# Optimization experiments

Measured on AMD Instinct MI355X. Metric: run time of the kernel, lower is better.

Reference implementation:

```python
import jax, jax.numpy as jnp
import numpy as np

DIM_IN = 768
HEADS = 12
DIM_HEAD = 64
SCALE = DIM_HEAD ** (-0.5)


def setup_inputs() -> dict:
    key = jax.random.key(0)
    k_x, k_qkv, k_out = jax.random.split(key, 3)
    B, N = 2, 2048
    x = jax.random.normal(k_x, (B, N, DIM_IN), dtype=jnp.float32)
    # w_qkv: Linear(dim_in, 3*heads*dim_head, bias=False); stored as [in, out] for x @ W
    w_qkv = jax.random.normal(k_qkv, (DIM_IN, HEADS * 3 * DIM_HEAD), dtype=jnp.float32) * (DIM_IN ** -0.5)
    # merge_heads Linear(heads*dim_head, dim_in) with bias
    w_out = jax.random.normal(k_out, (HEADS * DIM_HEAD, DIM_IN), dtype=jnp.float32) * ((HEADS * DIM_HEAD) ** -0.5)
    b_out = jnp.zeros((DIM_IN,), dtype=jnp.float32)
    return {"x": x, "w_qkv": w_qkv, "w_out": w_out, "b_out": b_out}


def reference(x, w_qkv, w_out, b_out):
    B, N, _ = x.shape
    qkv = x @ w_qkv                                   # [B, N, H*3*Dh]
    qkv = qkv.reshape(B, N, HEADS, 3, DIM_HEAD)       # matches torch reshape order
    q = jnp.transpose(qkv[:, :, :, 0, :], (0, 2, 1, 3))  # [B, H, N, Dh]
    k = jnp.transpose(qkv[:, :, :, 1, :], (0, 2, 1, 3))
    v = jnp.transpose(qkv[:, :, :, 2, :], (0, 2, 1, 3))
    scores = jnp.einsum("bhnd,bhmd->bhnm", q, k) * SCALE  # full N x N score matrix
    attn = jax.nn.softmax(scores, axis=-1)
    ctx = jnp.einsum("bhnm,bhmd->bhnd", attn, v)          # [B, H, N, Dh]
    heads = jnp.transpose(ctx, (0, 2, 1, 3)).reshape(B, N, HEADS * DIM_HEAD)
    out = heads @ w_out + b_out                            # dropout is identity at inference
    return out
```

## Files before the change

### kernel.cpp

```cpp
#include <hip/hip_runtime.h>

#define SEQ   2048
#define BATCH 2
#define DIN   768
#define NH    12
#define DH    64
#define QKVN  (NH*3*DH)
#define NBH   (BATCH*NH)
#define QSCALE 0.18033688011112042f

typedef __attribute__((ext_vector_type(8))) short short8;
typedef __attribute__((ext_vector_type(4))) float float4v;

__device__ __forceinline__ ushort f2bf(float f) {
  union { float f; uint u; } v; v.f = f;
  return (ushort)((v.u + 0x7fffu + ((v.u >> 16) & 1u)) >> 16);
}

__device__ __forceinline__ void gld_lds16(const void* g, void* l) {
  __builtin_amdgcn_global_load_lds(
      (__attribute__((address_space(1))) unsigned int*)(g),
      (__attribute__((address_space(3))) unsigned int*)(l), 16, 0, 0);
}

__global__ __launch_bounds__(256) void cvt_all(const float* __restrict__ X,
                                               ushort* __restrict__ Xb,
                                               const float* __restrict__ Wq,
                                               ushort* __restrict__ WqT,
                                               const float* __restrict__ Wo,
                                               ushort* __restrict__ WoT) {
  __shared__ float tile[32][33];
  const int bid = blockIdx.x;
  if (bid < 3072) {
    int i = bid * 256 + threadIdx.x;
    float4 v = ((const float4*)X)[i];
    ushort4 o;
    o.x = f2bf(v.x); o.y = f2bf(v.y); o.z = f2bf(v.z); o.w = f2bf(v.w);
    ((ushort4*)Xb)[i] = o;
    return;
  }
  const float* W; ushort* WT; int Ndim, idx;
  if (bid < 3072 + 1728) { idx = bid - 3072; W = Wq; WT = WqT; Ndim = QKVN; }
  else                   { idx = bid - 4800; W = Wo; WT = WoT; Ndim = DIN;  }
  const int bx = idx % (DIN / 32), by = idx / (DIN / 32);
  const int r0 = bx * 32, c0 = by * 32;
  const int tx = threadIdx.x & 31, tg = threadIdx.x >> 5;
#pragma unroll
  for (int i = 0; i < 4; ++i) {
    int r = tg + i * 8;
    tile[r][tx] = W[(size_t)(r0 + r) * Ndim + c0 + tx];
  }
  __syncthreads();
#pragma unroll
  for (int i = 0; i < 4; ++i) {
    int c = tg + i * 8;
    WT[(size_t)(c0 + c) * DIN + r0 + tx] = f2bf(tile[tx][c]);
  }
}

#define GEMM_CORE(Abf, BT)                                                     \
  __shared__ ushort As[8192];                                                  \
  __shared__ ushort Bs[8192];                                                  \
  const int t = threadIdx.x;                                                   \
  const int lane = t & 63, wid = t >> 6;                                       \
  const int wr = wid >> 1, wc = wid & 1;                                       \
  const int m0 = blockIdx.x * 128, n0 = blockIdx.y * 128;                      \
  float4v acc[4][4] = {};                                                      \
  for (int k0 = 0; k0 < DIN; k0 += 64) {                                       \
    __syncthreads();                                                           \
    _Pragma("unroll")                                                          \
    for (int i = 0; i < 4; ++i) {                                              \
      int s   = t + i * 256;                                                   \
      int sub = s >> 7, kss = (s >> 6) & 1, l = s & 63;                        \
      int row = sub * 16 + (l & 15);                                           \
      int kc  = kss * 32 + (l >> 4) * 8;                                       \
      int lb  = (i * 256 + wid * 64) * 8;           \
      gld_lds16(&Abf[(size_t)(m0 + row) * DIN + k0 + kc], &As[lb]);            \
      gld_lds16(&BT[(size_t)(n0 + row) * DIN + k0 + kc], &Bs[lb]);             \
    }                                                                          \
    __syncthreads();                                                           \
    _Pragma("unroll")                                                          \
    for (int ks = 0; ks < 2; ++ks) {                                           \
      short8 a[4], b[4];                                                       \
      _Pragma("unroll")                                                        \
      for (int mi = 0; mi < 4; ++mi)                                           \
        a[mi] = *(const short8*)&As[(((wr * 4 + mi) * 2 + ks) * 64 + lane) * 8];\
      _Pragma("unroll")                                                        \
      for (int ni = 0; ni < 4; ++ni)                                           \
        b[ni] = *(const short8*)&Bs[(((wc * 4 + ni) * 2 + ks) * 64 + lane) * 8];\
      _Pragma("unroll")                                                        \
      for (int mi = 0; mi < 4; ++mi)                                           \
        _Pragma("unroll")                                                      \
        for (int ni = 0; ni < 4; ++ni)                                         \
          acc[mi][ni] = __builtin_amdgcn_mfma_f32_16x16x32_bf16(               \
              a[mi], b[ni], acc[mi][ni], 0, 0, 0);                             \
    }                                                                          \
  }

__global__ __launch_bounds__(256) void gemm_qkv(const ushort* __restrict__ Abf,
                                                const ushort* __restrict__ BT,
                                                ushort* __restrict__ Q,
                                                ushort* __restrict__ K,
                                                ushort* __restrict__ Vt) {
  GEMM_CORE(Abf, BT)
  __syncthreads();
  ushort* scr = &As[wid * 1024];
  const int eL = lane & 15, eH = lane >> 4;
  const int cb64  = n0 + wc * 64;
  const int h     = cb64 / 192;
  const int which = (cb64 % 192) / 64;
  const int mbase = m0 + wr * 64;
  if (which == 2) {
#pragma unroll
    for (int ni = 0; ni < 4; ++ni) {
      const int d0 = ni * 16 + eL;
#pragma unroll
      for (int mi = 0; mi < 4; ++mi) {
        const int mrow = mbase + mi * 16 + eH * 4;
        const int bb = mrow >> 11, n = mrow & (SEQ - 1);
        const int bhv = bb * NH + h;
        ushort4 pk;
        pk.x = f2bf(acc[mi][ni][0]); pk.y = f2bf(acc[mi][ni][1]);
        pk.z = f2bf(acc[mi][ni][2]); pk.w = f2bf(acc[mi][ni][3]);
        *(ushort4*)&Vt[((size_t)bhv * DH + d0) * SEQ + n] = pk;
      }
    }
  } else {
    ushort* dst = (which == 0) ? Q : K;
    const float sc = (which == 0) ? QSCALE : 1.0f;
    const int rr = lane >> 2;
    const int rb = (lane & 3) ^ (rr >> 2);
    const int roff = rr * 64 + rb * 16;
#pragma unroll
    for (int mi = 0; mi < 4; ++mi) {
      const int mrow = mbase + mi * 16;
      const int bb = mrow >> 11, nb = mrow & (SEQ - 1);
#pragma unroll
      for (int ni = 0; ni < 4; ++ni) {
        const int sb = ((ni ^ eH) & 3) * 16;
#pragma unroll
        for (int r = 0; r < 4; ++r)
          scr[(eH * 4 + r) * 64 + sb + eL] = f2bf(acc[mi][ni][r] * sc);
      }
      asm volatile("s_waitcnt lgkmcnt(0)" ::: "memory");
      short8 v0 = *(const short8*)&scr[roff];
      short8 v1 = *(const short8*)&scr[roff + 8];
      ushort* gp = dst + ((size_t)(bb * NH + h) * SEQ + nb) * DH + lane * 16;
      *(short8*)&gp[0] = v0;
      *(short8*)&gp[8] = v1;
      asm volatile("s_waitcnt lgkmcnt(0)" ::: "memory");
    }
  }
}

__global__ __launch_bounds__(256) void gemm_out(const ushort* __restrict__ Abf,
                                                const ushort* __restrict__ BT,
                                                const float* __restrict__ bias,
                                                float* __restrict__ Out) {
  GEMM_CORE(Abf, BT)
#pragma unroll
  for (int ni = 0; ni < 4; ++ni) {
    const int c = n0 + wc * 64 + ni * 16 + (lane & 15);
    const float bv = bias[c];
#pragma unroll
    for (int mi = 0; mi < 4; ++mi) {
      const int mrow = m0 + wr * 64 + mi * 16 + (lane >> 4) * 4;
#pragma unroll
      for (int r = 0; r < 4; ++r)
        Out[(size_t)(mrow + r) * DIN + c] = acc[mi][ni][r] + bv;
    }
  }
}

__global__ __launch_bounds__(256) void attn(const ushort* __restrict__ Q,
                                            const ushort* __restrict__ K,
                                            const ushort* __restrict__ Vt,
                                            ushort* __restrict__ CTX) {
  __shared__ ushort Ks[2][4096];
  __shared__ ushort Vs[2][4096];
  __shared__ ushort ps[4][1024];
  const int t = threadIdx.x, lane = t & 63, wid = t >> 6;
  const int lo = lane & 15, hi = lane >> 4;
  const int bid = blockIdx.x;
  const int bh = bid % NBH;
  const int q0 = (bid / NBH) * 64 + wid * 16;
  const size_t base = (size_t)bh * SEQ * DH;
  ushort* myps = ps[wid];

  int kvoff[4][2];
#pragma unroll
  for (int ns = 0; ns < 4; ++ns)
#pragma unroll
    for (int ks = 0; ks < 2; ++ks) {
      int row = ns * 16 + lo;
      kvoff[ns][ks] = (row * 128 + ks * 64 + hi * 16) ^ ((row & 7) << 4);
    }
  int pwoff[4], proff[2];
#pragma unroll
  for (int ns = 0; ns < 4; ++ns)
    pwoff[ns] = (lo * 128 + ns * 32 + hi * 8) ^ ((lo & 7) << 4);
#pragma unroll
  for (int ks = 0; ks < 2; ++ks)
    proff[ks] = (lo * 128 + ks * 64 + hi * 16) ^ ((lo & 7) << 4);

  const int c0i = t, c1i = t + 256;
  const int g0 = c0i ^ ((c0i >> 3) & 7), g1 = c1i ^ ((c1i >> 3) & 7);
  const int lb0 = (wid * 64) * 8, lb1 = (256 + wid * 64) * 8;
  const ushort* kp0 = K + base + g0 * 8;
  const ushort* kp1 = K + base + g1 * 8;
  const ushort* vp0 = Vt + (size_t)bh * DH * SEQ + (size_t)(g0 >> 3) * SEQ + (g0 & 7) * 8;
  const ushort* vp1 = Vt + (size_t)bh * DH * SEQ + (size_t)(g1 >> 3) * SEQ + (g1 & 7) * 8;

  short8 qf[2];
#pragma unroll
  for (int ks = 0; ks < 2; ++ks)
    qf[ks] = *(const short8*)&Q[base + (size_t)(q0 + lo) * DH + ks * 32 + hi * 8];

  float4v Ot[4] = {};
  float mrun = -1e30f, lrun = 0.f;

  gld_lds16(kp0, &Ks[0][lb0]);
  gld_lds16(kp1, &Ks[0][lb1]);
  gld_lds16(vp0, &Vs[0][lb0]);
  gld_lds16(vp1, &Vs[0][lb1]);
  kp0 += 64 * DH; kp1 += 64 * DH; vp0 += 64; vp1 += 64;
  __syncthreads();

  const int NT = SEQ / 64;
  for (int kt = 0; kt < NT; ++kt) {
    const int cur = kt & 1, nb = cur ^ 1;
    const char* Kl = (const char*)&Ks[cur][0];
    const char* Vl = (const char*)&Vs[cur][0];
    if (kt + 1 < NT) {
      gld_lds16(kp0, &Ks[nb][lb0]);
      gld_lds16(kp1, &Ks[nb][lb1]);
      gld_lds16(vp0, &Vs[nb][lb0]);
      gld_lds16(vp1, &Vs[nb][lb1]);
      kp0 += 64 * DH; kp1 += 64 * DH; vp0 += 64; vp1 += 64;
    }
    float4v st[4];
#pragma unroll
    for (int ns = 0; ns < 4; ++ns) {
      st[ns] = (float4v){0.f, 0.f, 0.f, 0.f};
#pragma unroll
      for (int ks = 0; ks < 2; ++ks) {
        short8 kf = *(const short8*)(Kl + kvoff[ns][ks]);
        st[ns] = __builtin_amdgcn_mfma_f32_16x16x32_bf16(kf, qf[ks], st[ns], 0, 0, 0);
      }
    }
    float mx = fmaxf(fmaxf(fmaxf(st[0][0], st[0][1]), fmaxf(st[0][2], st[0][3])),
                     fmaxf(fmaxf(st[1][0], st[1][1]), fmaxf(st[1][2], st[1][3])));
    mx = fmaxf(mx, fmaxf(fmaxf(fmaxf(st[2][0], st[2][1]), fmaxf(st[2][2], st[2][3])),
                         fmaxf(fmaxf(st[3][0], st[3][1]), fmaxf(st[3][2], st[3][3]))));
    mx = fmaxf(mx, __shfl_xor(mx, 16));
    mx = fmaxf(mx, __shfl_xor(mx, 32));
    if (!__all(mx <= mrun + 8.0f)) {
      float mnew  = fmaxf(mrun, mx);
      float alpha = exp2f(mrun - mnew);
      lrun *= alpha;
#pragma unroll
      for (int ns = 0; ns < 4; ++ns)
#pragma unroll
        for (int r = 0; r < 4; ++r) Ot[ns][r] *= alpha;
      mrun = mnew;
    }
    float p[4][4];
    float rs = 0.f;
#pragma unroll
    for (int ns = 0; ns < 4; ++ns)
#pragma unroll
      for (int r = 0; r < 4; ++r) {
        p[ns][r] = exp2f(st[ns][r] - mrun);
        rs += p[ns][r];
      }
    rs += __shfl_xor(rs, 16);
    rs += __shfl_xor(rs, 32);
    lrun += rs;
#pragma unroll
    for (int ns = 0; ns < 4; ++ns) {
      uint2 d2;
      d2.x = __builtin_amdgcn_perm(__float_as_uint(p[ns][1]),
                                   __float_as_uint(p[ns][0]), 0x07060302u);
      d2.y = __builtin_amdgcn_perm(__float_as_uint(p[ns][3]),
                                   __float_as_uint(p[ns][2]), 0x07060302u);
      *(uint2*)((char*)myps + pwoff[ns]) = d2;
    }
    asm volatile("s_waitcnt lgkmcnt(0)" ::: "memory");
    short8 pf[2];
#pragma unroll
    for (int ks = 0; ks < 2; ++ks)
      pf[ks] = *(const short8*)((char*)myps + proff[ks]);
    __builtin_amdgcn_s_setprio(1);
#pragma unroll
    for (int ns = 0; ns < 4; ++ns)
#pragma unroll
      for (int ks = 0; ks < 2; ++ks) {
        short8 vf = *(const short8*)(Vl + kvoff[ns][ks]);
        Ot[ns] = __builtin_amdgcn_mfma_f32_16x16x32_bf16(vf, pf[ks], Ot[ns], 0, 0, 0);
      }
    __builtin_amdgcn_s_setprio(0);
    __syncthreads();
  }
  const int bb = bh / NH, h = bh % NH;
  const float inv = 1.0f / lrun;
  const int n = q0 + lo;
#pragma unroll
  for (int ns = 0; ns < 4; ++ns) {
    ushort4 o;
    o.x = f2bf(Ot[ns][0] * inv); o.y = f2bf(Ot[ns][1] * inv);
    o.z = f2bf(Ot[ns][2] * inv); o.w = f2bf(Ot[ns][3] * inv);
    *(ushort4*)&CTX[(size_t)(bb * SEQ + n) * DIN + h * DH + ns * 16 + hi * 4] = o;
  }
}

extern "C" void kernel_launch(void* const* d_in, const int* in_sizes, int n_in,
                              void* d_out, int out_size, void* d_ws, size_t ws_size,
                              hipStream_t stream) {
  const float* x     = (const float*)d_in[0];
  const float* w_qkv = (const float*)d_in[1];
  const float* w_out = (const float*)d_in[2];
  const float* b_out = (const float*)d_in[3];
  float* out = (float*)d_out;

  ushort* ws = (ushort*)d_ws;
  const size_t nX   = (size_t)BATCH * SEQ * DIN;
  const size_t nWq  = (size_t)DIN * QKVN;
  const size_t nWo  = (size_t)DIN * DIN;
  const size_t nQKV = (size_t)BATCH * NH * SEQ * DH;

  ushort* xb   = ws;
  ushort* wqT  = xb + nX;
  ushort* woT  = wqT + nWq;
  ushort* Qb   = woT + nWo;
  ushort* Kb   = Qb + nQKV;
  ushort* Vt   = Kb + nQKV;
  ushort* CTX  = Vt + nQKV;

  cvt_all<<<dim3(5376), 256, 0, stream>>>(x, xb, w_qkv, wqT, w_out, woT);
  gemm_qkv<<<dim3(BATCH * SEQ / 128, QKVN / 128), 256, 0, stream>>>(
      xb, wqT, Qb, Kb, Vt);
  attn<<<dim3(SEQ / 64 * NBH), 256, 0, stream>>>(Qb, Kb, Vt, CTX);
  gemm_out<<<dim3(BATCH * SEQ / 128, DIN / 128), 256, 0, stream>>>(
      CTX, woT, b_out, out);
}
```

Baseline: 208.9 us.

## Retile output GEMM to 64x64 blocks, add attn occupancy hint, use raw exp/rcp

The output projection GEMM now uses its own 64x64 tile kernel instead of the shared 128x128 core, which quadruples the block count (768 instead of 192) so the GPU's compute units are better filled. The attention kernel gains a launch bound requesting 3 waves per SIMD. Its exp2f and the final division are replaced with raw v_exp_f32 and v_rcp_f32 inline assembly. The small GEMM tiles lower data reuse and use a single-buffered loop, and the raw instructions skip denormal and range handling.

```diff
diff --git a/kernel.cpp b/kernel.cpp
--- a/kernel.cpp
+++ b/kernel.cpp
@@ -15,6 +15,13 @@
 __device__ __forceinline__ ushort f2bf(float f) {
   union { float f; uint u; } v; v.f = f;
   return (ushort)((v.u + 0x7fffu + ((v.u >> 16) & 1u)) >> 16);
+}
+
+__device__ __forceinline__ float fexp2(float x) {
+  float r; asm("v_exp_f32 %0, %1" : "=v"(r) : "v"(x)); return r;
+}
+__device__ __forceinline__ float frcp(float x) {
+  float r; asm("v_rcp_f32 %0, %1" : "=v"(r) : "v"(x)); return r;
 }
 
 __device__ __forceinline__ void gld_lds16(const void* g, void* l) {
@@ -157,14 +164,50 @@
                                                 const ushort* __restrict__ BT,
                                                 const float* __restrict__ bias,
                                                 float* __restrict__ Out) {
-  GEMM_CORE(Abf, BT)
-#pragma unroll
-  for (int ni = 0; ni < 4; ++ni) {
-    const int c = n0 + wc * 64 + ni * 16 + (lane & 15);
+  __shared__ ushort As[4096];
+  __shared__ ushort Bs[4096];
+  const int t = threadIdx.x;
+  const int lane = t & 63, wid = t >> 6;
+  const int wr = wid >> 1, wc = wid & 1;
+  const int m0 = blockIdx.x * 64, n0 = blockIdx.y * 64;
+  float4v acc[2][2] = {};
+  for (int k0 = 0; k0 < DIN; k0 += 64) {
+    __syncthreads();
+#pragma unroll
+    for (int i = 0; i < 2; ++i) {
+      int s   = t + i * 256;
+      int sub = s >> 7, kss = (s >> 6) & 1, l = s & 63;
+      int row = sub * 16 + (l & 15);
+      int kc  = kss * 32 + (l >> 4) * 8;
+      int lb  = (i * 256 + wid * 64) * 8;
+      gld_lds16(&Abf[(size_t)(m0 + row) * DIN + k0 + kc], &As[lb]);
+      gld_lds16(&BT[(size_t)(n0 + row) * DIN + k0 + kc], &Bs[lb]);
+    }
+    __syncthreads();
+#pragma unroll
+    for (int ks = 0; ks < 2; ++ks) {
+      short8 a[2], b[2];
+#pragma unroll
+      for (int mi = 0; mi < 2; ++mi)
+        a[mi] = *(const short8*)&As[(((wr * 2 + mi) * 2 + ks) * 64 + lane) * 8];
+#pragma unroll
+      for (int ni = 0; ni < 2; ++ni)
+        b[ni] = *(const short8*)&Bs[(((wc * 2 + ni) * 2 + ks) * 64 + lane) * 8];
+#pragma unroll
+      for (int mi = 0; mi < 2; ++mi)
+#pragma unroll
+        for (int ni = 0; ni < 2; ++ni)
+          acc[mi][ni] = __builtin_amdgcn_mfma_f32_16x16x32_bf16(
+              a[mi], b[ni], acc[mi][ni], 0, 0, 0);
+    }
+  }
+#pragma unroll
+  for (int ni = 0; ni < 2; ++ni) {
+    const int c = n0 + wc * 32 + ni * 16 + (lane & 15);
     const float bv = bias[c];
 #pragma unroll
-    for (int mi = 0; mi < 4; ++mi) {
-      const int mrow = m0 + wr * 64 + mi * 16 + (lane >> 4) * 4;
+    for (int mi = 0; mi < 2; ++mi) {
+      const int mrow = m0 + wr * 32 + mi * 16 + (lane >> 4) * 4;
 #pragma unroll
       for (int r = 0; r < 4; ++r)
         Out[(size_t)(mrow + r) * DIN + c] = acc[mi][ni][r] + bv;
@@ -172,10 +215,10 @@
   }
 }
 
-__global__ __launch_bounds__(256) void attn(const ushort* __restrict__ Q,
-                                            const ushort* __restrict__ K,
-                                            const ushort* __restrict__ Vt,
-                                            ushort* __restrict__ CTX) {
+__global__ __launch_bounds__(256, 3) void attn(const ushort* __restrict__ Q,
+                                               const ushort* __restrict__ K,
+                                               const ushort* __restrict__ Vt,
+                                               ushort* __restrict__ CTX) {
   __shared__ ushort Ks[2][4096];
   __shared__ ushort Vs[2][4096];
   __shared__ ushort ps[4][1024];
@@ -256,7 +299,7 @@
     mx = fmaxf(mx, __shfl_xor(mx, 32));
     if (!__all(mx <= mrun + 8.0f)) {
       float mnew  = fmaxf(mrun, mx);
-      float alpha = exp2f(mrun - mnew);
+      float alpha = fexp2(mrun - mnew);
       lrun *= alpha;
 #pragma unroll
       for (int ns = 0; ns < 4; ++ns)
@@ -270,7 +313,7 @@
     for (int ns = 0; ns < 4; ++ns)
 #pragma unroll
       for (int r = 0; r < 4; ++r) {
-        p[ns][r] = exp2f(st[ns][r] - mrun);
+        p[ns][r] = fexp2(st[ns][r] - mrun);
         rs += p[ns][r];
       }
     rs += __shfl_xor(rs, 16);
@@ -302,7 +345,7 @@
     __syncthreads();
   }
   const int bb = bh / NH, h = bh % NH;
-  const float inv = 1.0f / lrun;
+  const float inv = frcp(lrun);
   const int n = q0 + lo;
 #pragma unroll
   for (int ns = 0; ns < 4; ++ns) {
@@ -340,6 +383,6 @@
   gemm_qkv<<<dim3(BATCH * SEQ / 128, QKVN / 128), 256, 0, stream>>>(
       xb, wqT, Qb, Kb, Vt);
   attn<<<dim3(SEQ / 64 * NBH), 256, 0, stream>>>(Qb, Kb, Vt, CTX);
-  gemm_out<<<dim3(BATCH * SEQ / 128, DIN / 128), 256, 0, stream>>>(
+  gemm_out<<<dim3(BATCH * SEQ / 64, DIN / 64), 256, 0, stream>>>(
       CTX, woT, b_out, out);
 }
```

After: 187.9 us. 1.11x faster.
